# Kernel optimization log

Hardware: AMD Instinct MI355X
Metric: run time of the kernel (lower is better)

Reference implementation:

```python
import jax, jax.numpy as jnp
import numpy as np

N_NODES = 100_000
N_EDGES = 1_600_000
NUM_BASIS = 10
MAX_RADIUS = 5.0
NUM_NEIGHBORS = 10.0


def _sph_harm_lmax2(u):
    # u: [E,3] unit vectors. e3nn real spherical harmonics, lmax=2,
    # normalization='component' (each l-block has per-component unit variance).
    x, y, z = u[:, 0], u[:, 1], u[:, 2]
    s3 = jnp.sqrt(3.0)
    s5 = jnp.sqrt(5.0)
    s15 = jnp.sqrt(15.0)
    return jnp.stack([
        jnp.ones_like(x),                      # l=0
        s3 * x, s3 * y, s3 * z,                # l=1
        s15 * x * z,                           # l=2
        s15 * x * y,
        s5 * (y * y - 0.5 * (x * x + z * z)),
        s15 * y * z,
        0.5 * s15 * (z * z - x * x),
    ], axis=-1)                                # [E,9]


def _soft_one_hot_smooth_finite(r):
    # e3nn soft_one_hot_linspace(r, 0, max_radius, num_basis, 'smooth_finite', cutoff=True)
    vals = jnp.linspace(0.0, MAX_RADIUS, NUM_BASIS + 2)
    step = vals[1] - vals[0]
    vals = vals[1:-1]
    d = (r[:, None] - vals[None, :]) / step    # [E,num_basis]
    inside = jnp.abs(d) < 1.0
    d2 = jnp.where(inside, d * d, 0.0)
    y = 1.14136 * jnp.exp(2.0) * jnp.exp(-1.0 / (1.0 - d2))
    return jnp.where(inside, y, 0.0)


def setup_inputs() -> dict:
    key = jax.random.key(0)
    k1, k2, k3, k4, k5, k6 = jax.random.split(key, 6)
    return {
        "pos": jax.random.normal(k1, (N_NODES, 3), dtype=jnp.float32),
        "node_feats": jax.random.normal(k2, (N_NODES, 9), dtype=jnp.float32),
        "W1": jax.random.normal(k3, (NUM_BASIS, 16), dtype=jnp.float32),
        "W2": jax.random.normal(k4, (16, 3), dtype=jnp.float32),
        "edge_src": jax.random.randint(k5, (N_EDGES,), 0, N_NODES, dtype=jnp.int32),
        "edge_dst": jax.random.randint(k6, (N_EDGES,), 0, N_NODES, dtype=jnp.int32),
    }


def reference(pos, node_feats, W1, W2, edge_src, edge_dst):
    # gather: per-edge geometry
    edge_vec = pos[edge_dst] - pos[edge_src]          # [E,3]
    r = jnp.linalg.norm(edge_vec, axis=-1)            # [E]
    u = edge_vec / (r[:, None] + 1e-12)
    sh = _sph_harm_lmax2(u)                           # [E,9]

    # radial embedding -> small MLP -> per-edge tensor-product weights (weight_numel=3)
    emb = _soft_one_hot_smooth_finite(r) * jnp.sqrt(jnp.float32(NUM_BASIS))
    h = jax.nn.relu(emb @ W1 / jnp.sqrt(jnp.float32(NUM_BASIS))) * jnp.sqrt(2.0)
    w = h @ W2 / jnp.sqrt(16.0)                       # [E,3]

    # FullyConnectedTensorProduct('1x0e+1x1o+1x2e', sh, '1x0e'), shared_weights=False
    # paths: 0e*0e->0e, 1o*1o->0e, 2e*2e->0e ; w3j(l,l,0)=I/sqrt(2l+1); fan-in 3 paths.
    x1 = node_feats[edge_src]                         # [E,9]
    path_s = x1[:, 0] * sh[:, 0]
    path_p = jnp.sum(x1[:, 1:4] * sh[:, 1:4], axis=-1) / jnp.sqrt(3.0)
    path_d = jnp.sum(x1[:, 4:9] * sh[:, 4:9], axis=-1) / jnp.sqrt(5.0)
    msg = (w[:, 0] * path_s + w[:, 1] * path_p + w[:, 2] * path_d) / jnp.sqrt(3.0)

    # scatter-aggregate messages to destination nodes
    node_out = jax.ops.segment_sum(msg, edge_dst, num_segments=N_NODES)
    node_out = node_out / jnp.sqrt(jnp.float32(NUM_NEIGHBORS))
    return node_out[:, None]                          # [N,1] scalar ('1x0e') per node
```

## Files before the change

### kernel.cpp

```cpp
#include <hip/hip_runtime.h>
#include <math.h>

#define N_NODES 100000
#define N_EDGES 1600000

#define BUCKETS 32
#define GSPLIT 16
#define BUCKET_NODES (N_NODES / BUCKETS)
#define NSEG (BUCKETS * GSPLIT)
#define CAP 4096
#define CPAD 32

#define LUTN 512
#define LUT_SCALE 102.4f

#define PACK_BLOCKS ((N_NODES + 255) / 256)
#define LUT_BLOCKS  ((LUTN + 1 + 255) / 256)
#define NQ (N_EDGES / 4)
#define MSG_BLOCKS ((NQ + 255) / 256)

typedef _Float16 half8 __attribute__((ext_vector_type(8)));

__device__ __forceinline__ unsigned int pack_entry(int local, float m) {
    _Float16 h = (_Float16)m;
    unsigned short u;
    __builtin_memcpy(&u, &h, 2);
    return ((unsigned int)local << 16) | u;
}
__device__ __forceinline__ float entry_msg(unsigned int e) {
    unsigned short u = (unsigned short)(e & 0xFFFFu);
    _Float16 h;
    __builtin_memcpy(&h, &u, 2);
    return (float)h;
}

__device__ __forceinline__ float4 radial_w(float r, const float* W1, const float* W2) {
    const float q = r * 2.2f;
    const int   k = (int)floorf(q);
    int   b0 = k - 1, b1 = k;
    const float d0 = q - (float)k;
    const float d1 = d0 - 1.0f;
    const float A = 8.43357307f;
    float e0 = 0.0f, e1 = 0.0f;
    if (b0 >= 0 && b0 < 10) {
        const float dd = d0 * d0;
        if (dd < 1.0f) e0 = A * expf(-1.0f / (1.0f - dd));
    }
    if (b1 >= 0 && b1 < 10) {
        const float dd = d1 * d1;
        if (dd < 1.0f) e1 = A * expf(-1.0f / (1.0f - dd));
    }
    b0 = (b0 >= 0 && b0 < 10) ? b0 : 0;
    b1 = (b1 >= 0 && b1 < 10) ? b1 : 0;
    float acc0 = 0.0f, acc1 = 0.0f, acc2 = 0.0f;
#pragma unroll
    for (int j = 0; j < 16; ++j) {
        const float hj = fmaxf(e0 * W1[b0 * 16 + j] + e1 * W1[b1 * 16 + j], 0.0f);
        acc0 = fmaf(hj, W2[j * 3 + 0], acc0);
        acc1 = fmaf(hj, W2[j * 3 + 1], acc1);
        acc2 = fmaf(hj, W2[j * 3 + 2], acc2);
    }
    const float FINAL = 0.06454972243679028f;
    return make_float4(acc0 * FINAL, acc1 * FINAL, acc2 * FINAL, 0.0f);
}

__global__ __launch_bounds__(256) void pack_kernel(
    const float* __restrict__ pos,
    const float* __restrict__ feats,
    const float* __restrict__ W1,
    const float* __restrict__ W2,
    half8* __restrict__ srcw,
    int*   __restrict__ counters,
    float4* __restrict__ lut)
{
    if (blockIdx.x >= PACK_BLOCKS) {
        const int i = (blockIdx.x - PACK_BLOCKS) * 256 + threadIdx.x;
        if (i <= LUTN) lut[i] = radial_w((float)i * (5.0f / (float)LUTN), W1, W2);
        return;
    }
    const int i = blockIdx.x * blockDim.x + threadIdx.x;
    if (i < NSEG * CPAD) counters[i] = 0;
    if (i >= N_NODES) return;
    const float* p = pos + 3 * i;
    const float* f = feats + 9 * i;
    half8 a, b;
    a[0] = (_Float16)p[0]; a[1] = (_Float16)p[1]; a[2] = (_Float16)p[2];
    a[3] = (_Float16)f[0]; a[4] = (_Float16)f[1]; a[5] = (_Float16)f[2];
    a[6] = (_Float16)f[3]; a[7] = (_Float16)f[4];
    b[0] = (_Float16)f[5]; b[1] = (_Float16)f[6]; b[2] = (_Float16)f[7];
    b[3] = (_Float16)f[8]; b[4] = (_Float16)0; b[5] = (_Float16)0;
    b[6] = (_Float16)0;    b[7] = (_Float16)0;
    srcw[2 * i + 0] = a;
    srcw[2 * i + 1] = b;
}

__device__ __forceinline__ float edge_msg_lut(
    const half8 ra, const half8 rb, const half8 pd,
    const float4* __restrict__ sLUT)
{
    const float vx = (float)pd[0] - (float)ra[0];
    const float vy = (float)pd[1] - (float)ra[1];
    const float vz = (float)pd[2] - (float)ra[2];

    const float r   = sqrtf(vx * vx + vy * vy + vz * vz);
    const float inv = 1.0f / (r + 1e-12f);
    const float x = vx * inv, y = vy * inv, z = vz * inv;

    const float s3  = 1.7320508075688772f;
    const float s5  = 2.23606797749979f;
    const float s15 = 3.872983346207417f;
    const float sh1 = s3 * x;
    const float sh2 = s3 * y;
    const float sh3 = s3 * z;
    const float sh4 = s15 * x * z;
    const float sh5 = s15 * x * y;
    const float sh6 = s5 * (y * y - 0.5f * (x * x + z * z));
    const float sh7 = s15 * y * z;
    const float sh8 = 0.5f * s15 * (z * z - x * x);

    float t = r * LUT_SCALE;
    int   i = (int)t;
    i = (i < LUTN) ? i : (LUTN - 1);
    const float fr = t - (float)i;
    const float4 wa = sLUT[i];
    const float4 wb = sLUT[i + 1];
    const float w0 = fmaf(fr, wb.x - wa.x, wa.x);
    const float w1 = fmaf(fr, wb.y - wa.y, wa.y);
    const float w2 = fmaf(fr, wb.z - wa.z, wa.z);

    const float path_s = (float)ra[3];
    const float path_p = ((float)ra[4] * sh1 + (float)ra[5] * sh2
                        + (float)ra[6] * sh3) * 0.5773502691896258f;
    const float path_d = ((float)ra[7] * sh4 + (float)rb[0] * sh5
                        + (float)rb[1] * sh6 + (float)rb[2] * sh7
                        + (float)rb[3] * sh8) * 0.4472135954999579f;

    return w0 * path_s + w1 * path_p + w2 * path_d;
}

__global__ __launch_bounds__(256) void msg_part_kernel(
    const half8* __restrict__ srcw,
    const float4* __restrict__ lut,
    const int4* __restrict__ src4,
    const int4* __restrict__ dst4,
    int*  __restrict__ counters,
    unsigned int* __restrict__ segs)
{
    __shared__ float4 sLUT[LUTN + 1];
    __shared__ int cnt[BUCKETS];
    __shared__ int basesm[BUCKETS];
    const int t = threadIdx.x;
    for (int i = t; i <= LUTN; i += 256) sLUT[i] = lut[i];
    if (t < BUCKETS) cnt[t] = 0;
    __syncthreads();

    const int q = blockIdx.x * 256 + t;
    const bool valid = q < NQ;
    int4 s4 = make_int4(0, 0, 0, 0), d4 = make_int4(0, 0, 0, 0);
    if (valid) { s4 = src4[q]; d4 = dst4[q]; }
    const int si[4] = { s4.x, s4.y, s4.z, s4.w };
    const int di[4] = { d4.x, d4.y, d4.z, d4.w };

    half8 ra[4], rb[4], pa[4];
#pragma unroll
    for (int i = 0; i < 4; ++i) {
        ra[i] = srcw[2 * si[i] + 0];
        rb[i] = srcw[2 * si[i] + 1];
        pa[i] = srcw[2 * di[i] + 0];
    }

    float m[4]; int bk[4], lo[4], rank[4];
#pragma unroll
    for (int i = 0; i < 4; ++i) {
        m[i]  = edge_msg_lut(ra[i], rb[i], pa[i], sLUT);
        bk[i] = di[i] / BUCKET_NODES;
        lo[i] = di[i] - bk[i] * BUCKET_NODES;
        rank[i] = valid ? atomicAdd(&cnt[bk[i]], 1) : 0;
    }
    __syncthreads();

    const int g = blockIdx.x & (GSPLIT - 1);
    if (t < BUCKETS)
        basesm[t] = atomicAdd(&counters[(t * GSPLIT + g) * CPAD], cnt[t]);
    __syncthreads();

    if (valid) {
#pragma unroll
        for (int i = 0; i < 4; ++i) {
            const int slot = basesm[bk[i]] + rank[i];
            if (slot < CAP)
                segs[(size_t)(bk[i] * GSPLIT + g) * CAP + slot] =
                    pack_entry(lo[i], m[i]);
        }
    }
}

__global__ __launch_bounds__(256) void scatter_kernel(
    const int* __restrict__ counters,
    const unsigned int* __restrict__ segs,
    float* __restrict__ slabs)
{
    __shared__ float acc[BUCKET_NODES];
    const int seg = blockIdx.x;
    const int t = threadIdx.x;
    for (int i = t; i < BUCKET_NODES; i += 256) acc[i] = 0.0f;
    __syncthreads();

    int count = counters[seg * CPAD];
    if (count > CAP) count = CAP;
    const unsigned int* sp = segs + (size_t)seg * CAP;
    const uint4* sp4 = (const uint4*)sp;
    const int n4 = count >> 2;
    for (int i = t; i < n4; i += 256) {
        const uint4 pr = sp4[i];
        atomicAdd(&acc[pr.x >> 16], entry_msg(pr.x));
        atomicAdd(&acc[pr.y >> 16], entry_msg(pr.y));
        atomicAdd(&acc[pr.z >> 16], entry_msg(pr.z));
        atomicAdd(&acc[pr.w >> 16], entry_msg(pr.w));
    }
    const int tail = count & 3;
    if (t < tail) {
        const unsigned int pr = sp[(n4 << 2) + t];
        atomicAdd(&acc[pr >> 16], entry_msg(pr));
    }
    __syncthreads();

    float* slab = slabs + (size_t)seg * BUCKET_NODES;
    for (int i = t; i < BUCKET_NODES; i += 256) slab[i] = acc[i];
}

__global__ __launch_bounds__(256) void reduce_kernel(
    const float* __restrict__ slabs, float* __restrict__ out)
{
    const int n = blockIdx.x * blockDim.x + threadIdx.x;
    if (n >= N_NODES) return;
    const int b = n / BUCKET_NODES;
    const int i = n - b * BUCKET_NODES;
    const float* sl = slabs + ((size_t)b * GSPLIT) * BUCKET_NODES + i;
    float sum = 0.0f;
#pragma unroll
    for (int g = 0; g < GSPLIT; ++g) sum += sl[(size_t)g * BUCKET_NODES];
    out[n] = sum;
}

__global__ __launch_bounds__(256) void edge_kernel_direct(
    const float* __restrict__ pos,
    const float* __restrict__ node_feats,
    const float* __restrict__ W1,
    const float* __restrict__ W2,
    const int*   __restrict__ edge_src,
    const int*   __restrict__ edge_dst,
    float* __restrict__ out)
{
    const int e = blockIdx.x * blockDim.x + threadIdx.x;
    if (e >= N_EDGES) return;

    const int src = edge_src[e];
    const int dst = edge_dst[e];
    const float* ps = pos + 3 * src;
    const float* pdp = pos + 3 * dst;
    const float* xf = node_feats + 9 * src;

    const float vx = pdp[0] - ps[0];
    const float vy = pdp[1] - ps[1];
    const float vz = pdp[2] - ps[2];
    const float r   = sqrtf(vx * vx + vy * vy + vz * vz);
    const float inv = 1.0f / (r + 1e-12f);
    const float x = vx * inv, y = vy * inv, z = vz * inv;

    const float s3  = 1.7320508075688772f;
    const float s5  = 2.23606797749979f;
    const float s15 = 3.872983346207417f;
    const float4 w = radial_w(r, W1, W2);
    const float path_s = xf[0];
    const float path_p = (xf[1] * s3 * x + xf[2] * s3 * y + xf[3] * s3 * z)
                         * 0.5773502691896258f;
    const float path_d = (xf[4] * s15 * x * z + xf[5] * s15 * x * y
                        + xf[6] * s5 * (y * y - 0.5f * (x * x + z * z))
                        + xf[7] * s15 * y * z
                        + xf[8] * 0.5f * s15 * (z * z - x * x))
                         * 0.4472135954999579f;
    unsafeAtomicAdd(out + dst, w.x * path_s + w.y * path_p + w.z * path_d);
}

extern "C" void kernel_launch(void* const* d_in, const int* in_sizes, int n_in,
                              void* d_out, int out_size, void* d_ws, size_t ws_size,
                              hipStream_t stream) {
    const float* pos        = (const float*)d_in[0];
    const float* node_feats = (const float*)d_in[1];
    const float* W1         = (const float*)d_in[2];
    const float* W2         = (const float*)d_in[3];
    const int*   edge_src   = (const int*)d_in[4];
    const int*   edge_dst   = (const int*)d_in[5];
    float* out = (float*)d_out;

    const size_t srcw_bytes = (size_t)N_NODES * 2 * sizeof(half8);
    const size_t lut_bytes  = (size_t)(LUTN + 1) * sizeof(float4);
    const size_t lut_pad    = (lut_bytes + 63) & ~(size_t)63;
    const size_t cnt_bytes  = (size_t)NSEG * CPAD * sizeof(int);
    const size_t seg_bytes  = (size_t)NSEG * CAP * sizeof(unsigned int);
    const size_t slab_bytes = (size_t)NSEG * BUCKET_NODES * sizeof(float);
    const size_t need = srcw_bytes + lut_pad + cnt_bytes + seg_bytes + slab_bytes;

    if (ws_size >= need) {
        char* w = (char*)d_ws;
        half8*  srcw = (half8*)w;          w += srcw_bytes;
        float4* lut  = (float4*)w;         w += lut_pad;
        int*    cnts = (int*)w;            w += cnt_bytes;
        unsigned int* segs = (unsigned int*)w;  w += seg_bytes;
        float*  slabs = (float*)w;

        pack_kernel<<<PACK_BLOCKS + LUT_BLOCKS, 256, 0, stream>>>(
            pos, node_feats, W1, W2, srcw, cnts, lut);
        msg_part_kernel<<<MSG_BLOCKS, 256, 0, stream>>>(
            srcw, lut, (const int4*)edge_src, (const int4*)edge_dst, cnts, segs);
        scatter_kernel<<<NSEG, 256, 0, stream>>>(cnts, segs, slabs);
        reduce_kernel<<<(N_NODES + 255) / 256, 256, 0, stream>>>(slabs, out);
    } else {
        hipMemsetAsync(out, 0, N_NODES * sizeof(float), stream);
        edge_kernel_direct<<<(N_EDGES + 255) / 256, 256, 0, stream>>>(
            pos, node_feats, W1, W2, edge_src, edge_dst, out);
    }
}
```

Baseline: 116.0 us.

## Use finer destination buckets and write scatter results directly to output

Destination buckets are reshaped from 32 buckets × 16 group-splits into 250 buckets of 400 nodes, each with a single segment. Each scatter block now owns a whole bucket and writes its shared-memory accumulator straight to the output. This removes the slab buffer and the separate reduce kernel, which cuts one launch and the slab write-and-reread traffic. In exchange, every message block issues 250 global counter atomics instead of 32, each counter is shared by all blocks, the scatter launch shrinks to 250 blocks with more shared-memory atomic contention per slot, and the segment capacity is raised to hold about 6400 entries per bucket.

```diff
diff --git a/kernel.cpp b/kernel.cpp
--- a/kernel.cpp
+++ b/kernel.cpp
@@ -4,11 +4,10 @@
 #define N_NODES 100000
 #define N_EDGES 1600000
 
-#define BUCKETS 32
-#define GSPLIT 16
-#define BUCKET_NODES (N_NODES / BUCKETS)
-#define NSEG (BUCKETS * GSPLIT)
-#define CAP 4096
+#define BUCKETS 250
+#define BUCKET_NODES 400
+#define NSEG BUCKETS
+#define CAP 8192
 #define CPAD 32
 
 #define LUTN 512
@@ -179,9 +178,8 @@
     }
     __syncthreads();
 
-    const int g = blockIdx.x & (GSPLIT - 1);
     if (t < BUCKETS)
-        basesm[t] = atomicAdd(&counters[(t * GSPLIT + g) * CPAD], cnt[t]);
+        basesm[t] = atomicAdd(&counters[t * CPAD], cnt[t]);
     __syncthreads();
 
     if (valid) {
@@ -189,8 +187,7 @@
         for (int i = 0; i < 4; ++i) {
             const int slot = basesm[bk[i]] + rank[i];
             if (slot < CAP)
-                segs[(size_t)(bk[i] * GSPLIT + g) * CAP + slot] =
-                    pack_entry(lo[i], m[i]);
+                segs[(size_t)bk[i] * CAP + slot] = pack_entry(lo[i], m[i]);
         }
     }
 }
@@ -198,7 +195,7 @@
 __global__ __launch_bounds__(256) void scatter_kernel(
     const int* __restrict__ counters,
     const unsigned int* __restrict__ segs,
-    float* __restrict__ slabs)
+    float* __restrict__ out)
 {
     __shared__ float acc[BUCKET_NODES];
     const int seg = blockIdx.x;
@@ -225,22 +222,8 @@
     }
     __syncthreads();
 
-    float* slab = slabs + (size_t)seg * BUCKET_NODES;
-    for (int i = t; i < BUCKET_NODES; i += 256) slab[i] = acc[i];
-}
-
-__global__ __launch_bounds__(256) void reduce_kernel(
-    const float* __restrict__ slabs, float* __restrict__ out)
-{
-    const int n = blockIdx.x * blockDim.x + threadIdx.x;
-    if (n >= N_NODES) return;
-    const int b = n / BUCKET_NODES;
-    const int i = n - b * BUCKET_NODES;
-    const float* sl = slabs + ((size_t)b * GSPLIT) * BUCKET_NODES + i;
-    float sum = 0.0f;
-#pragma unroll
-    for (int g = 0; g < GSPLIT; ++g) sum += sl[(size_t)g * BUCKET_NODES];
-    out[n] = sum;
+    float* o = out + seg * BUCKET_NODES;
+    for (int i = t; i < BUCKET_NODES; i += 256) o[i] = acc[i];
 }
 
 __global__ __launch_bounds__(256) void edge_kernel_direct(
@@ -299,23 +282,20 @@
     const size_t lut_pad    = (lut_bytes + 63) & ~(size_t)63;
     const size_t cnt_bytes  = (size_t)NSEG * CPAD * sizeof(int);
     const size_t seg_bytes  = (size_t)NSEG * CAP * sizeof(unsigned int);
-    const size_t slab_bytes = (size_t)NSEG * BUCKET_NODES * sizeof(float);
-    const size_t need = srcw_bytes + lut_pad + cnt_bytes + seg_bytes + slab_bytes;
+    const size_t need = srcw_bytes + lut_pad + cnt_bytes + seg_bytes;
 
     if (ws_size >= need) {
         char* w = (char*)d_ws;
         half8*  srcw = (half8*)w;          w += srcw_bytes;
         float4* lut  = (float4*)w;         w += lut_pad;
         int*    cnts = (int*)w;            w += cnt_bytes;
-        unsigned int* segs = (unsigned int*)w;  w += seg_bytes;
-        float*  slabs = (float*)w;
+        unsigned int* segs = (unsigned int*)w;
 
         pack_kernel<<<PACK_BLOCKS + LUT_BLOCKS, 256, 0, stream>>>(
             pos, node_feats, W1, W2, srcw, cnts, lut);
         msg_part_kernel<<<MSG_BLOCKS, 256, 0, stream>>>(
             srcw, lut, (const int4*)edge_src, (const int4*)edge_dst, cnts, segs);
-        scatter_kernel<<<NSEG, 256, 0, stream>>>(cnts, segs, slabs);
-        reduce_kernel<<<(N_NODES + 255) / 256, 256, 0, stream>>>(slabs, out);
+        scatter_kernel<<<NSEG, 256, 0, stream>>>(cnts, segs, out);
     } else {
         hipMemsetAsync(out, 0, N_NODES * sizeof(float), stream);
         edge_kernel_direct<<<(N_EDGES + 255) / 256, 256, 0, stream>>>(
```

Result: slower. 139.8 us (+20.5%).
